# Optimization experiments

Hardware: AMD Instinct MI355X
Metric: run time of the kernel (lower is better)

Reference implementation:

```python
import jax, jax.numpy as jnp
import numpy as np

B, S, D, H = 4, 2048, 1024, 4096
EPS = 1e-5

def _layernorm(x, g, b):
    mu = jnp.mean(x, axis=-1, keepdims=True)
    var = jnp.mean(jnp.square(x - mu), axis=-1, keepdims=True)
    return (x - mu) * jax.lax.rsqrt(var + EPS) * g + b

def setup_inputs() -> dict:
    key = jax.random.key(0)
    ks = jax.random.split(key, 8)
    s = lambda d: 1.0 / np.sqrt(d)
    return {
        "x": jax.random.normal(ks[0], (B, S, D), jnp.float32),
        "Wq": jax.random.normal(ks[1], (D, D), jnp.float32) * s(D),
        "bq": jnp.zeros((D,), jnp.float32),
        "Wk": jax.random.normal(ks[2], (D, D), jnp.float32) * s(D),
        "bk": jnp.zeros((D,), jnp.float32),
        "Wv": jax.random.normal(ks[3], (D, D), jnp.float32) * s(D),
        "bv": jnp.zeros((D,), jnp.float32),
        "Wo": jax.random.normal(ks[4], (D, D), jnp.float32) * s(D),
        "bo": jnp.zeros((D,), jnp.float32),
        "g1": jnp.ones((D,), jnp.float32),
        "be1": jnp.zeros((D,), jnp.float32),
        "g2": jnp.ones((D,), jnp.float32),
        "be2": jnp.zeros((D,), jnp.float32),
        "W1": jax.random.normal(ks[5], (D, H), jnp.float32) * s(D),
        "b1": jnp.zeros((H,), jnp.float32),
        "W2": jax.random.normal(ks[6], (H, D), jnp.float32) * s(H),
        "b2": jnp.zeros((D,), jnp.float32),
    }

def reference(x, Wq, bq, Wk, bk, Wv, bv, Wo, bo, g1, be1, g2, be2, W1, b1, W2, b2):
    # pre-norm self-attention + residual
    xn = _layernorm(x, g1, be1)
    q = xn @ Wq + bq            # [B,S,D]
    k = xn @ Wk + bk
    v = xn @ Wv + bv
    scale = 1.0 / jnp.sqrt(jnp.float32(D))
    scores = jnp.einsum("bsd,btd->bst", q, k) * scale  # [B,S,S]
    attn = jax.nn.softmax(scores, axis=-1)
    attn_out = jnp.einsum("bst,btd->bsd", attn, v) @ Wo + bo
    x = x + attn_out
    # pre-norm MLP + residual
    xn2 = _layernorm(x, g2, be2)
    ffn = jax.nn.relu(xn2 @ W1 + b1) @ W2 + b2
    out = x + ffn
    return out, attn
```

## Files before the change

kernel.cpp:

```cpp
#include <hip/hip_runtime.h>
#include <hip/hip_bf16.h>


typedef __bf16 bf16_t;
typedef __bf16 bf16x8 __attribute__((ext_vector_type(8)));
typedef float  f32x4  __attribute__((ext_vector_type(4)));

#define EPI_QKV            0
#define EPI_BF16_SCALE     1
#define EPI_BF16           3
#define EPI_F32_BIAS_RES   4
#define EPI_BF16_RELU_BIAS 5

__device__ __forceinline__ void gl_lds16(const bf16_t* g, void* l) {
  __builtin_amdgcn_global_load_lds(
      (const __attribute__((address_space(1))) void*)g,
      (__attribute__((address_space(3))) void*)l, 16, 0, 0);
}

template<int BM, int EPI>
__global__ __launch_bounds__(512, 2)
void gemm8p(const bf16_t* __restrict__ A, const bf16_t* __restrict__ B,
            float* __restrict__ Cf, bf16_t* __restrict__ Cb,
            const float* __restrict__ bias,
            int M, int N, int K, long sAb, long sBb, long sCb, float scale)
{
  constexpr int BN  = 256;
  constexpr int WTM = BM / 2;
  constexpr int MF  = WTM / 16;
  constexpr int NF  = 4;
  constexpr int LA  = BM / 128;
  constexpr int LB  = 2;
  constexpr int L   = LA + LB;
  constexpr int L0  = 2;
  constexpr int SBUF = (BM + BN) * 64;
  constexpr int W   = 2 * L;
  __shared__ __align__(16) char lds[4 * SBUF];

  const int tid = threadIdx.x;
  const int l   = tid & 63;
  const int w   = tid >> 6;
  const int wm  = w >> 2;
  const int wn  = w & 3;

  const int nx = gridDim.x, ny = gridDim.y;
  const int tot = nx * ny * gridDim.z;
  int id = blockIdx.x + nx * (blockIdx.y + ny * blockIdx.z);
  const int cpx = tot >> 3;
  int s = (id & 7) * cpx + (id >> 3);
  const int bx = s % nx; int rq = s / nx;
  const int by = rq % ny; const int bz = rq / ny;

  const bf16_t* Ab = A + (long)bz * sAb;
  const bf16_t* Bb = B + (long)bz * sBb;
  const int m0 = by * BM, n0 = bx * BN;
  const int NT = K >> 5;

  const int srow = w * 16 + (l >> 2);
  const int scol = ((l & 3) ^ ((l >> 3) & 3)) * 8;
  const bf16_t* srcA[LA]; const bf16_t* srcB[LB];
#pragma unroll
  for (int q = 0; q < LA; ++q) srcA[q] = Ab + (long)(m0 + q * 128 + srow) * K + scol;
#pragma unroll
  for (int q = 0; q < LB; ++q) srcB[q] = Bb + (long)(n0 + q * 128 + srow) * K + scol;
  const int ldsA = w * 1024;
  const int ldsB = BM * 64 + w * 1024;

  const int rA0 = wm * WTM + (l & 15);
  const int rB0 = wn * 64 + (l & 15);
  const int xoff = 16 * ((l >> 4) ^ ((l >> 1) & 3));

  f32x4 acc[MF][NF] = {};
  bf16x8 afr[MF / 2], bfr[NF];

#pragma unroll
  for (int d = 0; d < 3; ++d) {
    char* bufS = lds + d * SBUF;
    const long kst = (long)d * 32;
#pragma unroll
    for (int q = 0; q < LA; ++q) gl_lds16(srcA[q] + kst, bufS + ldsA + q * 8192);
#pragma unroll
    for (int q = 0; q < LB; ++q) gl_lds16(srcB[q] + kst, bufS + ldsB + q * 8192);
  }
  asm volatile("s_waitcnt vmcnt(%0)" :: "n"(W) : "memory");
  __builtin_amdgcn_s_barrier();
  __builtin_amdgcn_sched_barrier(0);

  for (int t = 0; t < NT; ++t) {
    const char* bufR = lds + (t & 3) * SBUF;
    char* bufS = lds + ((t + 3) & 3) * SBUF;
    const int tst = t + 3;
    const long kst = (long)((tst < NT) ? tst : (NT - 1)) * 32;

#pragma unroll
    for (int nf = 0; nf < NF; ++nf)
      bfr[nf] = *(const bf16x8*)(bufR + BM * 64 + (rB0 + nf * 16) * 64 + xoff);
#pragma unroll
    for (int mf = 0; mf < MF / 2; ++mf)
      afr[mf] = *(const bf16x8*)(bufR + (rA0 + mf * 16) * 64 + xoff);
#pragma unroll
    for (int q = 0; q < L0; ++q) {
      if (q < LA) gl_lds16(srcA[q] + kst, bufS + ldsA + q * 8192);
      else        gl_lds16(srcB[q - LA] + kst, bufS + ldsB + (q - LA) * 8192);
    }
    __builtin_amdgcn_s_barrier();
    __builtin_amdgcn_s_setprio(1);
#pragma unroll
    for (int mf = 0; mf < MF / 2; ++mf)
#pragma unroll
      for (int nf = 0; nf < NF; ++nf)
        acc[mf][nf] = __builtin_amdgcn_mfma_f32_16x16x32_bf16(afr[mf], bfr[nf], acc[mf][nf], 0, 0, 0);
    __builtin_amdgcn_s_setprio(0);
    __builtin_amdgcn_s_barrier();

#pragma unroll
    for (int mf = 0; mf < MF / 2; ++mf)
      afr[mf] = *(const bf16x8*)(bufR + (rA0 + (MF / 2 + mf) * 16) * 64 + xoff);
#pragma unroll
    for (int q = L0; q < L; ++q) {
      if (q < LA) gl_lds16(srcA[q] + kst, bufS + ldsA + q * 8192);
      else        gl_lds16(srcB[q - LA] + kst, bufS + ldsB + (q - LA) * 8192);
    }
    __builtin_amdgcn_s_barrier();
    __builtin_amdgcn_s_setprio(1);
#pragma unroll
    for (int mf = 0; mf < MF / 2; ++mf)
#pragma unroll
      for (int nf = 0; nf < NF; ++nf)
        acc[MF / 2 + mf][nf] = __builtin_amdgcn_mfma_f32_16x16x32_bf16(afr[mf], bfr[nf], acc[MF / 2 + mf][nf], 0, 0, 0);
    __builtin_amdgcn_s_setprio(0);
    asm volatile("s_waitcnt vmcnt(%0)" :: "n"(W) : "memory");
    __builtin_amdgcn_s_barrier();
    __builtin_amdgcn_sched_barrier(0);
  }
  asm volatile("s_waitcnt vmcnt(0)" ::: "memory");

  const int colB0 = n0 + wn * 64 + (l & 15);
  const int rowB0 = m0 + wm * WTM + ((l >> 4) << 2);
#pragma unroll
  for (int mi = 0; mi < MF; ++mi) {
#pragma unroll
    for (int ni = 0; ni < NF; ++ni) {
      const int col = colB0 + ni * 16;
#pragma unroll
      for (int j = 0; j < 4; ++j) {
        const int row = rowB0 + mi * 16 + j;
        const float v = acc[mi][ni][j];
        if constexpr (EPI == EPI_BF16_SCALE) {
          Cb[sCb * bz + (long)row * N + col] = (bf16_t)(v * scale);
        } else {
          const float u = v + bias[col];
          Cb[(long)row * N + col] = (bf16_t)(u > 0.f ? u : 0.f);
        }
      }
    }
  }
}

template<int EPI>
__global__ __launch_bounds__(512, 1)
void gemm128(const bf16_t* __restrict__ A, const bf16_t* __restrict__ B,
             float* __restrict__ Cf, bf16_t* __restrict__ Cb,
             const float* __restrict__ bias, const float* __restrict__ resid,
             int M, int N, int K, long sAb, long sBb, long sCb)
{
  constexpr int SBUF = 49152;
  __shared__ __align__(16) char lds[3 * SBUF];
  const int tid = threadIdx.x;
  const int l   = tid & 63;
  const int w   = tid >> 6;
  const int wm  = w >> 2, wn = w & 3;

  const int nx = gridDim.x, ny = gridDim.y;
  const int tot = nx * ny * gridDim.z;
  int id = blockIdx.x + nx * (blockIdx.y + ny * blockIdx.z);
  const int cpx = tot >> 3;
  int sid = (id & 7) * cpx + (id >> 3);
  const int bx = sid % nx; int rq = sid / nx;
  const int by = rq % ny; const int bz = rq / ny;

  const bf16_t* Ab = A + (long)bz * sAb;
  const bf16_t* Bb = B + (long)bz * sBb;
  const int m0 = by * 128, n0 = bx * 256;
  const int NT = K >> 6;

  const int scol = ((l & 7) ^ (l >> 3)) * 8;
  const bf16_t* srcA = Ab + (long)(m0 + 16 * w + (l >> 3)) * K + scol;
  const bf16_t* srcB = Bb + (long)(n0 + 32 * w + (l >> 3)) * K + scol;
  const int dA = w * 2048 + l * 16;
  const int dB = 16384 + w * 4096 + l * 16;

  const int rA = wm * 64 + (l & 15);
  const int rB = wn * 64 + (l & 15);
  const int xo = ((l >> 4) ^ (l & 7)) * 16;
  const int aoff = rA * 128 + xo;
  const int boff = 16384 + rB * 128 + xo;

  f32x4 acc[4][4] = {};
  bf16x8 af[4], bv[4];

  {
    char* b0 = lds; char* b1 = lds + SBUF;
#pragma unroll
    for (int q = 0; q < 2; ++q) gl_lds16(srcA + (long)q * 8 * K, b0 + dA + q * 1024);
#pragma unroll
    for (int q = 0; q < 4; ++q) gl_lds16(srcB + (long)q * 8 * K, b0 + dB + q * 1024);
#pragma unroll
    for (int q = 0; q < 2; ++q) gl_lds16(srcA + (long)q * 8 * K + 64, b1 + dA + q * 1024);
#pragma unroll
    for (int q = 0; q < 4; ++q) gl_lds16(srcB + (long)q * 8 * K + 64, b1 + dB + q * 1024);
  }
  asm volatile("s_waitcnt vmcnt(6)" ::: "memory");
  __builtin_amdgcn_s_barrier();
  __builtin_amdgcn_sched_barrier(0);

  int ir = 0, is = 2;
  for (int t = 0; t < NT; ++t) {
    const char* bufR = lds + ir * SBUF;
    char* bufS = lds + is * SBUF;
    const int tst = (t + 2 < NT) ? t + 2 : NT - 1;
    const long kst = (long)tst * 64;

#pragma unroll
    for (int nf = 0; nf < 4; ++nf) bv[nf] = *(const bf16x8*)(bufR + boff + nf * 2048);
#pragma unroll
    for (int mf = 0; mf < 4; ++mf) af[mf] = *(const bf16x8*)(bufR + aoff + mf * 2048);
    gl_lds16(srcA + kst,                 bufS + dA);
    gl_lds16(srcA + (long)8 * K + kst,   bufS + dA + 1024);
    gl_lds16(srcB + kst,                 bufS + dB);
    __builtin_amdgcn_s_barrier();
    __builtin_amdgcn_s_setprio(1);
#pragma unroll
    for (int mf = 0; mf < 4; ++mf)
#pragma unroll
      for (int nf = 0; nf < 4; ++nf)
        acc[mf][nf] = __builtin_amdgcn_mfma_f32_16x16x32_bf16(af[mf], bv[nf], acc[mf][nf], 0, 0, 0);
    __builtin_amdgcn_s_setprio(0);
    __builtin_amdgcn_s_barrier();

#pragma unroll
    for (int nf = 0; nf < 4; ++nf) bv[nf] = *(const bf16x8*)(bufR + ((boff + nf * 2048) ^ 64));
#pragma unroll
    for (int mf = 0; mf < 4; ++mf) af[mf] = *(const bf16x8*)(bufR + ((aoff + mf * 2048) ^ 64));
    gl_lds16(srcB + (long)8 * K + kst,   bufS + dB + 1024);
    gl_lds16(srcB + (long)16 * K + kst,  bufS + dB + 2048);
    gl_lds16(srcB + (long)24 * K + kst,  bufS + dB + 3072);
    __builtin_amdgcn_s_barrier();
    __builtin_amdgcn_s_setprio(1);
#pragma unroll
    for (int mf = 0; mf < 4; ++mf)
#pragma unroll
      for (int nf = 0; nf < 4; ++nf)
        acc[mf][nf] = __builtin_amdgcn_mfma_f32_16x16x32_bf16(af[mf], bv[nf], acc[mf][nf], 0, 0, 0);
    __builtin_amdgcn_s_setprio(0);
    asm volatile("s_waitcnt vmcnt(6)" ::: "memory");
    __builtin_amdgcn_s_barrier();
    __builtin_amdgcn_sched_barrier(0);
    ir = (ir == 2) ? 0 : ir + 1;
    is = (is == 2) ? 0 : is + 1;
  }
  asm volatile("s_waitcnt vmcnt(0)" ::: "memory");

  const int colB0 = n0 + wn * 64 + (l & 15);
  const int rowB0 = m0 + wm * 64 + ((l >> 4) << 2);
#pragma unroll
  for (int mi = 0; mi < 4; ++mi) {
#pragma unroll
    for (int ni = 0; ni < 4; ++ni) {
      const int col = colB0 + ni * 16;
#pragma unroll
      for (int j = 0; j < 4; ++j) {
        const int row = rowB0 + mi * 16 + j;
        const float v = acc[mi][ni][j];
        if constexpr (EPI == EPI_BF16) {
          Cb[sCb * bz + (long)row * N + col] = (bf16_t)v;
        } else {
          Cf[(long)row * N + col] = v + bias[col] + resid[(long)row * N + col];
        }
      }
    }
  }
}

__global__ __launch_bounds__(512, 2)
void gemm128_32(const bf16_t* __restrict__ A, const bf16_t* __restrict__ B,
                bf16_t* __restrict__ Cb, bf16_t* __restrict__ Cb2,
                bf16_t* __restrict__ Cb3,
                const float* __restrict__ bias, const float* __restrict__ bias2,
                const float* __restrict__ bias3, int M, int N, int K)
{
  constexpr int SBUF = 24576;
  __shared__ __align__(16) char lds[3 * SBUF];
  const int tid = threadIdx.x;
  const int l   = tid & 63;
  const int w   = tid >> 6;
  const int wm  = w >> 2, wn = w & 3;

  const int nx = gridDim.x, ny = gridDim.y;
  const int tot = nx * ny;
  int id = blockIdx.x + nx * blockIdx.y;
  const int cpx = tot >> 3;
  int sid = (id & 7) * cpx + (id >> 3);
  const int bx = sid % nx;
  const int by = sid / nx;

  const int m0 = by * 128, n0 = bx * 256;
  const int NT = K >> 5;

  const int srow = (l >> 2);
  const int scol = ((l & 3) ^ ((l >> 3) & 3)) * 8;
  const bf16_t* srcA = A + (long)(m0 + w * 16 + srow) * K + scol;
  const bf16_t* srcB0 = B + (long)(n0 + w * 32 + srow) * K + scol;
  const bf16_t* srcB1 = srcB0 + (long)16 * K;
  const int dA = w * 1024 + l * 16;
  const int dB = 8192 + w * 2048 + l * 16;

  const int rA = wm * 64 + (l & 15);
  const int rB = wn * 64 + (l & 15);
  const int xoff = 16 * ((l >> 4) ^ ((l >> 1) & 3));
  const int aoff = rA * 64 + xoff;
  const int boff = 8192 + rB * 64 + xoff;

  f32x4 acc[4][4] = {};
  bf16x8 af[4], bv[4];

  gl_lds16(srcA,       lds + dA);
  gl_lds16(srcB0,      lds + dB);
  gl_lds16(srcB1,      lds + dB + 1024);
  gl_lds16(srcA + 32,  lds + SBUF + dA);
  gl_lds16(srcB0 + 32, lds + SBUF + dB);
  gl_lds16(srcB1 + 32, lds + SBUF + dB + 1024);
  asm volatile("s_waitcnt vmcnt(3)" ::: "memory");
  __builtin_amdgcn_s_barrier();
  __builtin_amdgcn_sched_barrier(0);

  int ir = 0, is = 2;
  for (int t = 0; t < NT; ++t) {
    const char* bufR = lds + ir * SBUF;
    char* bufS = lds + is * SBUF;
    const long kst = (long)((t + 2 < NT) ? t + 2 : NT - 1) * 32;

#pragma unroll
    for (int nf = 0; nf < 4; ++nf) bv[nf] = *(const bf16x8*)(bufR + boff + nf * 1024);
#pragma unroll
    for (int mf = 0; mf < 4; ++mf) af[mf] = *(const bf16x8*)(bufR + aoff + mf * 1024);
    gl_lds16(srcA + kst, bufS + dA);
    gl_lds16(srcB0 + kst, bufS + dB);
    gl_lds16(srcB1 + kst, bufS + dB + 1024);
    __builtin_amdgcn_s_setprio(1);
#pragma unroll
    for (int mf = 0; mf < 4; ++mf)
#pragma unroll
      for (int nf = 0; nf < 4; ++nf)
        acc[mf][nf] = __builtin_amdgcn_mfma_f32_16x16x32_bf16(af[mf], bv[nf], acc[mf][nf], 0, 0, 0);
    __builtin_amdgcn_s_setprio(0);
    asm volatile("s_waitcnt vmcnt(3)" ::: "memory");
    __builtin_amdgcn_s_barrier();
    __builtin_amdgcn_sched_barrier(0);
    ir = (ir == 2) ? 0 : ir + 1;
    is = (is == 2) ? 0 : is + 1;
  }
  asm volatile("s_waitcnt vmcnt(0)" ::: "memory");

  const int colB0 = n0 + wn * 64 + (l & 15);
  const int rowB0 = m0 + wm * 64 + ((l >> 4) << 2);
#pragma unroll
  for (int mi = 0; mi < 4; ++mi) {
#pragma unroll
    for (int ni = 0; ni < 4; ++ni) {
      const int col = colB0 + ni * 16;
#pragma unroll
      for (int j = 0; j < 4; ++j) {
        const int row = rowB0 + mi * 16 + j;
        const float v = acc[mi][ni][j];
        if (col < 1024)      Cb [(long)row * 1024 + col]        = (bf16_t)(v + bias[col]);
        else if (col < 2048) Cb2[(long)row * 1024 + col - 1024] = (bf16_t)(v + bias2[col - 1024]);
        else                 Cb3[(long)row * 1024 + col - 2048] = (bf16_t)(v + bias3[col - 2048]);
      }
    }
  }
}

__global__ __launch_bounds__(256)
void transpose_bf(const bf16_t* __restrict__ V, bf16_t* __restrict__ VT)
{
  __shared__ __align__(16) bf16_t t[64][72];
  const int b = blockIdx.z;
  const int t0 = blockIdx.y * 64, d0 = blockIdx.x * 64;
  const int r = threadIdx.x >> 3;
  const int c = (threadIdx.x & 7) * 8;
  const bf16_t* src = V + ((long)b * 2048 + t0) * 1024 + d0;
#pragma unroll
  for (int h = 0; h < 2; ++h)
    *(bf16x8*)&t[r + 32 * h][c] = *(const bf16x8*)(src + (long)(r + 32 * h) * 1024 + c);
  __syncthreads();
  bf16_t* dst = VT + ((long)b * 1024 + d0) * 2048 + t0;
#pragma unroll
  for (int h = 0; h < 2; ++h) {
    const int d = r + 32 * h;
    bf16x8 o;
#pragma unroll
    for (int j = 0; j < 8; ++j) o[j] = t[c + j][d];
    *(bf16x8*)(dst + (long)d * 2048 + c) = o;
  }
}

__global__ __launch_bounds__(256)
void transpose_all(const float* __restrict__ Wq, const float* __restrict__ Wk,
                   const float* __restrict__ Wv, const float* __restrict__ Wo,
                   const float* __restrict__ W1, const float* __restrict__ W2,
                   bf16_t* __restrict__ WqkvT, bf16_t* __restrict__ WoT,
                   bf16_t* __restrict__ W1T, bf16_t* __restrict__ W2T)
{
  const int id = blockIdx.x;
  const float* W; bf16_t* WT; int R, C, cb, rb;
  if (id < 4096) {
    const int wsel = id >> 10, loc = id & 1023;
    cb = loc & 31; rb = loc >> 5; R = 1024; C = 1024;
    if (wsel == 0)      { W = Wq; WT = WqkvT; }
    else if (wsel == 1) { W = Wk; WT = WqkvT + 1024L * 1024; }
    else if (wsel == 2) { W = Wv; WT = WqkvT + 2048L * 1024; }
    else                { W = Wo; WT = WoT; }
  } else if (id < 8192) {
    const int loc = id - 4096;
    cb = loc & 127; rb = loc >> 7; R = 1024; C = 4096;
    W = W1; WT = W1T;
  } else {
    const int loc = id - 8192;
    cb = loc & 31; rb = loc >> 5; R = 4096; C = 1024;
    W = W2; WT = W2T;
  }
  __shared__ float t[32][33];
  const int c0 = cb * 32, r0 = rb * 32;
  const int tx = threadIdx.x & 31, ty = threadIdx.x >> 5;
#pragma unroll
  for (int i = 0; i < 32; i += 8)
    t[ty + i][tx] = W[(long)(r0 + ty + i) * C + c0 + tx];
  __syncthreads();
#pragma unroll
  for (int i = 0; i < 32; i += 8)
    WT[(long)(c0 + ty + i) * R + r0 + tx] = (bf16_t)t[tx][ty + i];
}

__global__ __launch_bounds__(256)
void ln_kernel(const float* __restrict__ x, const float* __restrict__ g,
               const float* __restrict__ be, bf16_t* __restrict__ out)
{
  const long row = blockIdx.x;
  const float4 v = *(const float4*)(x + row * 1024 + threadIdx.x * 4);
  float s  = v.x + v.y + v.z + v.w;
  float s2 = v.x * v.x + v.y * v.y + v.z * v.z + v.w * v.w;
  __shared__ float red[10];
  const int lane = threadIdx.x & 63, w = threadIdx.x >> 6;
#pragma unroll
  for (int off = 32; off; off >>= 1) {
    s  += __shfl_down(s, off);
    s2 += __shfl_down(s2, off);
  }
  if (lane == 0) { red[w] = s; red[4 + w] = s2; }
  __syncthreads();
  if (threadIdx.x == 0) {
    const float ts = red[0] + red[1] + red[2] + red[3];
    const float t2 = red[4] + red[5] + red[6] + red[7];
    const float mu = ts * (1.f / 1024.f);
    const float var = t2 * (1.f / 1024.f) - mu * mu;
    red[8] = mu;
    red[9] = rsqrtf(var + 1e-5f);
  }
  __syncthreads();
  const float mu = red[8], rinv = red[9];
  const int c = threadIdx.x * 4;
  const float4 gv = *(const float4*)(g + c);
  const float4 bvv = *(const float4*)(be + c);
  bf16_t* o = out + row * 1024 + c;
  o[0] = (bf16_t)((v.x - mu) * rinv * gv.x + bvv.x);
  o[1] = (bf16_t)((v.y - mu) * rinv * gv.y + bvv.y);
  o[2] = (bf16_t)((v.z - mu) * rinv * gv.z + bvv.z);
  o[3] = (bf16_t)((v.w - mu) * rinv * gv.w + bvv.w);
}

__global__ __launch_bounds__(256)
void softmax_kernel(float* __restrict__ sc, bf16_t* __restrict__ ab)
{
  const long row = blockIdx.x;
  const int t0 = threadIdx.x * 8;
  const bf16x8 v8 = *(const bf16x8*)(ab + row * 2048 + t0);
  float e[8];
#pragma unroll
  for (int j = 0; j < 8; ++j) e[j] = (float)v8[j];
  float mx = fmaxf(fmaxf(fmaxf(e[0], e[1]), fmaxf(e[2], e[3])),
                   fmaxf(fmaxf(e[4], e[5]), fmaxf(e[6], e[7])));
  __shared__ float red[4];
  __shared__ float bc[2];
  const int lane = threadIdx.x & 63, w = threadIdx.x >> 6;
#pragma unroll
  for (int off = 32; off; off >>= 1) mx = fmaxf(mx, __shfl_down(mx, off));
  if (lane == 0) red[w] = mx;
  __syncthreads();
  if (threadIdx.x == 0) bc[0] = fmaxf(fmaxf(red[0], red[1]), fmaxf(red[2], red[3]));
  __syncthreads();
  const float m = bc[0];
  float s = 0.f;
#pragma unroll
  for (int j = 0; j < 8; ++j) { e[j] = __expf(e[j] - m); s += e[j]; }
#pragma unroll
  for (int off = 32; off; off >>= 1) s += __shfl_down(s, off);
  __syncthreads();
  if (lane == 0) red[w] = s;
  __syncthreads();
  if (threadIdx.x == 0) bc[1] = 1.f / (red[0] + red[1] + red[2] + red[3]);
  __syncthreads();
  const float inv = bc[1];
  float4 oa, ob;
  oa.x = e[0] * inv; oa.y = e[1] * inv; oa.z = e[2] * inv; oa.w = e[3] * inv;
  ob.x = e[4] * inv; ob.y = e[5] * inv; ob.z = e[6] * inv; ob.w = e[7] * inv;
  *(float4*)(sc + row * 2048 + t0)     = oa;
  *(float4*)(sc + row * 2048 + t0 + 4) = ob;
  bf16x8 o8;
  o8[0] = (bf16_t)oa.x; o8[1] = (bf16_t)oa.y; o8[2] = (bf16_t)oa.z; o8[3] = (bf16_t)oa.w;
  o8[4] = (bf16_t)ob.x; o8[5] = (bf16_t)ob.y; o8[6] = (bf16_t)ob.z; o8[7] = (bf16_t)ob.w;
  *(bf16x8*)(ab + row * 2048 + t0) = o8;
}

extern "C" void kernel_launch(void* const* d_in, const int* in_sizes, int n_in,
                              void* d_out, int out_size, void* d_ws, size_t ws_size,
                              hipStream_t stream)
{
  const float* x   = (const float*)d_in[0];
  const float* Wq  = (const float*)d_in[1];
  const float* bq  = (const float*)d_in[2];
  const float* Wk  = (const float*)d_in[3];
  const float* bk  = (const float*)d_in[4];
  const float* Wv  = (const float*)d_in[5];
  const float* bv  = (const float*)d_in[6];
  const float* Wo  = (const float*)d_in[7];
  const float* bo  = (const float*)d_in[8];
  const float* g1  = (const float*)d_in[9];
  const float* be1 = (const float*)d_in[10];
  const float* g2  = (const float*)d_in[11];
  const float* be2 = (const float*)d_in[12];
  const float* W1  = (const float*)d_in[13];
  const float* b1  = (const float*)d_in[14];
  const float* W2  = (const float*)d_in[15];
  const float* b2  = (const float*)d_in[16];

  float* out   = (float*)d_out;
  float* attnF = out + 8192L * 1024;
  bf16_t* vB   = (bf16_t*)attnF;

  char* ws = (char*)d_ws;
  const size_t MB = 1024 * 1024;
  bf16_t* WqkvT = (bf16_t*)(ws + 0 * MB);
  bf16_t* WoT   = (bf16_t*)(ws + 6 * MB);
  bf16_t* W1T   = (bf16_t*)(ws + 8 * MB);
  bf16_t* W2T   = (bf16_t*)(ws + 16 * MB);
  bf16_t* xn    = (bf16_t*)(ws + 24 * MB);
  bf16_t* qB    = (bf16_t*)(ws + 40 * MB);
  bf16_t* kB    = (bf16_t*)(ws + 56 * MB);
  bf16_t* vT    = (bf16_t*)(ws + 72 * MB);
  bf16_t* atB   = (bf16_t*)(ws + 88 * MB);
  float*  x2    = (float* )(ws + 120 * MB);
  bf16_t* hB    = (bf16_t*)(ws + 56 * MB);

  transpose_all<<<12288, 256, 0, stream>>>(
      Wq, Wk, Wv, Wo, W1, W2, WqkvT, WoT, W1T, W2T);

  ln_kernel<<<8192, 256, 0, stream>>>(x, g1, be1, xn);

  gemm128_32<<<dim3(12, 64), 512, 0, stream>>>(
      xn, WqkvT, qB, kB, vB, bq, bk, bv, 8192, 3072, 1024);

  transpose_bf<<<dim3(16, 32, 4), 256, 0, stream>>>(vB, vT);

  gemm8p<256, EPI_BF16_SCALE><<<dim3(8, 8, 4), 512, 0, stream>>>(
      qB, kB, nullptr, atB, nullptr,
      2048, 2048, 1024, 2048L * 1024, 2048L * 1024, 2048L * 2048, 0.03125f);

  softmax_kernel<<<8192, 256, 0, stream>>>(attnF, atB);

  gemm128<EPI_BF16><<<dim3(4, 16, 4), 512, 0, stream>>>(
      atB, vT, nullptr, qB, nullptr, nullptr,
      2048, 1024, 2048, 2048L * 2048, 1024L * 2048, 2048L * 1024);

  gemm128<EPI_F32_BIAS_RES><<<dim3(4, 64, 1), 512, 0, stream>>>(
      qB, WoT, x2, nullptr, bo, x,
      8192, 1024, 1024, 0, 0, 0);

  ln_kernel<<<8192, 256, 0, stream>>>(x2, g2, be2, xn);

  gemm8p<256, EPI_BF16_RELU_BIAS><<<dim3(16, 32, 1), 512, 0, stream>>>(
      xn, W1T, nullptr, hB, b1,
      8192, 4096, 1024, 0, 0, 0, 1.f);
  gemm128<EPI_F32_BIAS_RES><<<dim3(4, 64, 1), 512, 0, stream>>>(
      hB, W2T, out, nullptr, b2, x2,
      8192, 1024, 4096, 0, 0, 0);
}
```

Measured before the change: 389.4 us.

## Prefetch next k-tile LDS fragments into registers across GEMM main loop

Restructures the GEMM main loop into two alternating steps with register double-buffering. The B fragments and first-half A fragments for k-tile t+1 are read from LDS during tile t, so LDS reads overlap the MFMA work instead of stalling before it. Global-to-LDS loads are split into an A pair and a B pair, one pair per half-step. In exchange, register pressure rises, the kernel is hardcoded to BM=256, and the number of k-tiles must be even.

```diff
diff --git a/kernel.cpp b/kernel.cpp
--- a/kernel.cpp
+++ b/kernel.cpp
@@ -6,7 +6,6 @@
 typedef __bf16 bf16x8 __attribute__((ext_vector_type(8)));
 typedef float  f32x4  __attribute__((ext_vector_type(4)));
 
-#define EPI_QKV            0
 #define EPI_BF16_SCALE     1
 #define EPI_BF16           3
 #define EPI_F32_BIAS_RES   4
@@ -25,16 +24,12 @@
             const float* __restrict__ bias,
             int M, int N, int K, long sAb, long sBb, long sCb, float scale)
 {
+  static_assert(BM == 256, "read-ahead body assumes MF=8");
   constexpr int BN  = 256;
   constexpr int WTM = BM / 2;
   constexpr int MF  = WTM / 16;
   constexpr int NF  = 4;
-  constexpr int LA  = BM / 128;
-  constexpr int LB  = 2;
-  constexpr int L   = LA + LB;
-  constexpr int L0  = 2;
   constexpr int SBUF = (BM + BN) * 64;
-  constexpr int W   = 2 * L;
   __shared__ __align__(16) char lds[4 * SBUF];
 
   const int tid = threadIdx.x;
@@ -58,11 +53,11 @@
 
   const int srow = w * 16 + (l >> 2);
   const int scol = ((l & 3) ^ ((l >> 3) & 3)) * 8;
-  const bf16_t* srcA[LA]; const bf16_t* srcB[LB];
-#pragma unroll
-  for (int q = 0; q < LA; ++q) srcA[q] = Ab + (long)(m0 + q * 128 + srow) * K + scol;
-#pragma unroll
-  for (int q = 0; q < LB; ++q) srcB[q] = Bb + (long)(n0 + q * 128 + srow) * K + scol;
+  const bf16_t* srcA[2]; const bf16_t* srcB[2];
+#pragma unroll
+  for (int q = 0; q < 2; ++q) srcA[q] = Ab + (long)(m0 + q * 128 + srow) * K + scol;
+#pragma unroll
+  for (int q = 0; q < 2; ++q) srcB[q] = Bb + (long)(n0 + q * 128 + srow) * K + scol;
   const int ldsA = w * 1024;
   const int ldsB = BM * 64 + w * 1024;
 
@@ -71,67 +66,74 @@
   const int xoff = 16 * ((l >> 4) ^ ((l >> 1) & 3));
 
   f32x4 acc[MF][NF] = {};
-  bf16x8 afr[MF / 2], bfr[NF];
+  bf16x8 a0[4], a1[4], bva[NF], bvb[NF];
 
 #pragma unroll
   for (int d = 0; d < 3; ++d) {
     char* bufS = lds + d * SBUF;
     const long kst = (long)d * 32;
 #pragma unroll
-    for (int q = 0; q < LA; ++q) gl_lds16(srcA[q] + kst, bufS + ldsA + q * 8192);
-#pragma unroll
-    for (int q = 0; q < LB; ++q) gl_lds16(srcB[q] + kst, bufS + ldsB + q * 8192);
-  }
-  asm volatile("s_waitcnt vmcnt(%0)" :: "n"(W) : "memory");
+    for (int q = 0; q < 2; ++q) gl_lds16(srcA[q] + kst, bufS + ldsA + q * 8192);
+#pragma unroll
+    for (int q = 0; q < 2; ++q) gl_lds16(srcB[q] + kst, bufS + ldsB + q * 8192);
+  }
+  asm volatile("s_waitcnt vmcnt(4)" ::: "memory");
   __builtin_amdgcn_s_barrier();
   __builtin_amdgcn_sched_barrier(0);
 
-  for (int t = 0; t < NT; ++t) {
+#pragma unroll
+  for (int mf = 0; mf < 4; ++mf)
+    a0[mf] = *(const bf16x8*)(lds + (rA0 + mf * 16) * 64 + xoff);
+#pragma unroll
+  for (int nf = 0; nf < NF; ++nf)
+    bva[nf] = *(const bf16x8*)(lds + BM * 64 + (rB0 + nf * 16) * 64 + xoff);
+
+  auto step = [&](int t, bf16x8 (&BV)[NF], bf16x8 (&BNx)[NF]) {
     const char* bufR = lds + (t & 3) * SBUF;
+    const char* bufN = lds + ((t + 1) & 3) * SBUF;
     char* bufS = lds + ((t + 3) & 3) * SBUF;
     const int tst = t + 3;
     const long kst = (long)((tst < NT) ? tst : (NT - 1)) * 32;
 
 #pragma unroll
+    for (int mf = 0; mf < 4; ++mf)
+      a1[mf] = *(const bf16x8*)(bufR + (rA0 + (4 + mf) * 16) * 64 + xoff);
+#pragma unroll
     for (int nf = 0; nf < NF; ++nf)
-      bfr[nf] = *(const bf16x8*)(bufR + BM * 64 + (rB0 + nf * 16) * 64 + xoff);
-#pragma unroll
-    for (int mf = 0; mf < MF / 2; ++mf)
-      afr[mf] = *(const bf16x8*)(bufR + (rA0 + mf * 16) * 64 + xoff);
-#pragma unroll
-    for (int q = 0; q < L0; ++q) {
-      if (q < LA) gl_lds16(srcA[q] + kst, bufS + ldsA + q * 8192);
-      else        gl_lds16(srcB[q - LA] + kst, bufS + ldsB + (q - LA) * 8192);
-    }
+      BNx[nf] = *(const bf16x8*)(bufN + BM * 64 + (rB0 + nf * 16) * 64 + xoff);
+    gl_lds16(srcA[0] + kst, bufS + ldsA);
+    gl_lds16(srcA[1] + kst, bufS + ldsA + 8192);
     __builtin_amdgcn_s_barrier();
     __builtin_amdgcn_s_setprio(1);
 #pragma unroll
-    for (int mf = 0; mf < MF / 2; ++mf)
+    for (int mf = 0; mf < 4; ++mf)
 #pragma unroll
       for (int nf = 0; nf < NF; ++nf)
-        acc[mf][nf] = __builtin_amdgcn_mfma_f32_16x16x32_bf16(afr[mf], bfr[nf], acc[mf][nf], 0, 0, 0);
+        acc[mf][nf] = __builtin_amdgcn_mfma_f32_16x16x32_bf16(a0[mf], BV[nf], acc[mf][nf], 0, 0, 0);
     __builtin_amdgcn_s_setprio(0);
     __builtin_amdgcn_s_barrier();
 
 #pragma unroll
-    for (int mf = 0; mf < MF / 2; ++mf)
-      afr[mf] = *(const bf16x8*)(bufR + (rA0 + (MF / 2 + mf) * 16) * 64 + xoff);
-#pragma unroll
-    for (int q = L0; q < L; ++q) {
-      if (q < LA) gl_lds16(srcA[q] + kst, bufS + ldsA + q * 8192);
-      else        gl_lds16(srcB[q - LA] + kst, bufS + ldsB + (q - LA) * 8192);
-    }
+    for (int mf = 0; mf < 4; ++mf)
+      a0[mf] = *(const bf16x8*)(bufN + (rA0 + mf * 16) * 64 + xoff);
+    gl_lds16(srcB[0] + kst, bufS + ldsB);
+    gl_lds16(srcB[1] + kst, bufS + ldsB + 8192);
     __builtin_amdgcn_s_barrier();
     __builtin_amdgcn_s_setprio(1);
 #pragma unroll
-    for (int mf = 0; mf < MF / 2; ++mf)
+    for (int mf = 0; mf < 4; ++mf)
 #pragma unroll
       for (int nf = 0; nf < NF; ++nf)
-        acc[MF / 2 + mf][nf] = __builtin_amdgcn_mfma_f32_16x16x32_bf16(afr[mf], bfr[nf], acc[MF / 2 + mf][nf], 0, 0, 0);
+        acc[4 + mf][nf] = __builtin_amdgcn_mfma_f32_16x16x32_bf16(a1[mf], BV[nf], acc[4 + mf][nf], 0, 0, 0);
     __builtin_amdgcn_s_setprio(0);
-    asm volatile("s_waitcnt vmcnt(%0)" :: "n"(W) : "memory");
+    asm volatile("s_waitcnt vmcnt(4)" ::: "memory");
     __builtin_amdgcn_s_barrier();
     __builtin_amdgcn_sched_barrier(0);
+  };
+
+  for (int t = 0; t < NT; t += 2) {
+    step(t,     bva, bvb);
+    step(t + 1, bvb, bva);
   }
   asm volatile("s_waitcnt vmcnt(0)" ::: "memory");
 
```

New measurement: 386.1 us (median of 2 runs). About the same (-0.8%).
